# Kernel tuning notes

Measured on AMD Instinct MI355X. Metric: run time of the kernel, lower is better.

The kernel has to match this reference:

```python
import jax, jax.numpy as jnp
import numpy as np

N = 100000      # num nodes
E = 800000      # num edges
IN = 128        # in_channels
OUT = 128       # out_channels
ALPHA = 0.5


def setup_inputs() -> dict:
    key = jax.random.key(0)
    k1, k2, k3, k4, k5, k6 = jax.random.split(key, 6)
    x = jax.random.normal(k1, (N, IN), dtype=jnp.float32)
    edge_index = jax.random.randint(k2, (2, E), 0, N, dtype=jnp.int32)
    # GCNConv linear weights (glorot-ish) and biases for both directions
    s = 1.0 / np.sqrt(IN)
    W_sd = jax.random.normal(k3, (IN, OUT), dtype=jnp.float32) * s
    b_sd = jnp.zeros((OUT,), dtype=jnp.float32)
    W_ds = jax.random.normal(k4, (IN, OUT), dtype=jnp.float32) * s
    b_ds = jnp.zeros((OUT,), dtype=jnp.float32)
    return {"x": x, "edge_index": edge_index, "W_sd": W_sd, "b_sd": b_sd,
            "W_ds": W_ds, "b_ds": b_ds}


def _dir_gcn_norm_weights(row, col, dtype):
    """edge_weight = out_deg_inv_sqrt[row] * in_deg_inv_sqrt[col] (unit input weights)."""
    ones = jnp.ones((row.shape[0],), dtype=dtype)
    in_deg = jax.ops.segment_sum(ones, col, num_segments=N)
    out_deg = jax.ops.segment_sum(ones, row, num_segments=N)
    in_inv = jnp.where(in_deg > 0, jax.lax.rsqrt(in_deg), 0.0).astype(dtype)
    out_inv = jnp.where(out_deg > 0, jax.lax.rsqrt(out_deg), 0.0).astype(dtype)
    return out_inv[row] * in_inv[col]


def _gcn_conv(x, W, b, src, dst, w):
    """GCNConv(normalize=False, add_self_loops=False): lin -> gather -> scale -> scatter-add -> +bias."""
    h = x @ W                                   # [N, OUT]
    msg = h[src] * w[:, None]                   # [E, OUT]
    return jax.ops.segment_sum(msg, dst, num_segments=N) + b


def reference(x, edge_index, W_sd, b_sd, W_ds, b_ds):
    row, col = edge_index[0], edge_index[1]
    # forward-direction norm (src->dst) and transposed-graph norm (edge_index.flip(0))
    w = _dir_gcn_norm_weights(row, col, x.dtype)
    w_t = _dir_gcn_norm_weights(col, row, x.dtype)
    # conv_dst_to_src uses transposed edges: source=col, dest=row
    x_in = _gcn_conv(x, W_ds, b_ds, col, row, w_t)
    # conv_src_to_dst uses original edges: source=row, dest=col
    x_out = _gcn_conv(x, W_sd, b_sd, row, col, w)
    return ALPHA * x_in + (1.0 - ALPHA) * x_out
```

## Files before the change

kernel.cpp:

```cpp
#include <hip/hip_runtime.h>

#define NN 100000
#define NE 800000
#define NI 1600000
#define NB 391
#define IPB 6250

#define GB_CVT 12500
#define GB_PW  128
#define GB_HIST 256

#define OFF_INV    0u
#define OFF_OFFS   800000u
#define OFF_BB     1600008u
#define OFF_HIST   1601600u
#define OFF_CSRC   2001984u
#define OFF_XB     8401984u
#define OFF_PAIRS  34001984u
#define OFF_WT     85201984u
#define OFF_BIAS   85267520u
#define OFF_TOT    85268032u

typedef short short8 __attribute__((ext_vector_type(8)));
typedef unsigned short u16x8 __attribute__((ext_vector_type(8)));
typedef float f32x4 __attribute__((ext_vector_type(4)));
typedef float f32x8 __attribute__((ext_vector_type(8)));

__device__ __forceinline__ unsigned short f2bf(float f) {
    unsigned u = __float_as_uint(f);
    u = (u + 0x7FFFu + ((u >> 16) & 1u)) >> 16;
    return (unsigned short)u;
}
__device__ __forceinline__ float b2f(unsigned short h) {
    return __uint_as_float(((unsigned)h) << 16);
}
__device__ __forceinline__ f32x8 bvec2f(u16x8 v) {
    f32x8 r;
#pragma unroll
    for (int i = 0; i < 8; ++i) r[i] = b2f(v[i]);
    return r;
}


__global__ __launch_bounds__(256) void k_prep(
    const float4* __restrict__ x4, ushort4* __restrict__ xb4,
    const float* __restrict__ Wds, const float* __restrict__ Wsd,
    const float* __restrict__ bds, const float* __restrict__ bsd,
    unsigned short* __restrict__ wt, float* __restrict__ bias,
    const int* __restrict__ ei, int* __restrict__ hist) {
    __shared__ int h[NB];
    int bid = blockIdx.x;
    if (bid < GB_CVT) {
        int i = bid * 256 + threadIdx.x;
        float4 v = x4[i];
        ushort4 o;
        o.x = f2bf(v.x); o.y = f2bf(v.y); o.z = f2bf(v.z); o.w = f2bf(v.w);
        xb4[i] = o;
        return;
    }
    if (bid < GB_CVT + GB_PW) {
        int id = (bid - GB_CVT) * 256 + threadIdx.x;
        int c = id & 127;
        int k = id >> 7;
        float v = (k < 128) ? Wds[k * 128 + c] : Wsd[(k - 128) * 128 + c];
        wt[c * 256 + k] = f2bf(v);
        if (k == 0) bias[c] = 0.5f * (bds[c] + bsd[c]);
        return;
    }
    int hb = bid - GB_CVT - GB_PW;
    for (int k = threadIdx.x; k < NB; k += 256) h[k] = 0;
    __syncthreads();
    int base = hb * IPB;
    for (int t = threadIdx.x; t < IPB; t += 256) {
        int i = base + t;
        int key = (i < NE) ? ei[i] : (NN + ei[i]);
        atomicAdd(&h[key >> 9], 1);
    }
    __syncthreads();
    for (int k = threadIdx.x; k < NB; k += 256) hist[k * 256 + hb] = h[k];
}

__global__ __launch_bounds__(256) void k_red(const int* __restrict__ hist,
                                             int* __restrict__ tot) {
    __shared__ int s[256];
    int k = blockIdx.x;
    s[threadIdx.x] = hist[k * 256 + threadIdx.x];
    __syncthreads();
    for (int st = 128; st > 0; st >>= 1) {
        if (threadIdx.x < st) s[threadIdx.x] += s[threadIdx.x + st];
        __syncthreads();
    }
    if (threadIdx.x == 0) tot[k] = s[0];
}

__global__ __launch_bounds__(512) void k_scan_tot(const int* __restrict__ tot,
                                                  int* __restrict__ bb) {
    __shared__ int sA[512], sB[512];
    int tid = threadIdx.x;
    int v = (tid < NB) ? tot[tid] : 0;
    sA[tid] = v;
    __syncthreads();
    int *src = sA, *dst = sB;
    for (int st = 1; st < 512; st <<= 1) {
        dst[tid] = src[tid] + ((tid >= st) ? src[tid - st] : 0);
        __syncthreads();
        int* tp = src; src = dst; dst = tp;
    }
    if (tid <= NB) bb[tid] = (tid > 0) ? src[tid - 1] : 0;
}

__global__ __launch_bounds__(256) void k_rebase(int* __restrict__ hist,
                                                const int* __restrict__ bb) {
    __shared__ int sA[256], sB[256];
    int k = blockIdx.x, tid = threadIdx.x;
    int v = hist[k * 256 + tid];
    sA[tid] = v;
    __syncthreads();
    int *src = sA, *dst = sB;
    for (int st = 1; st < 256; st <<= 1) {
        dst[tid] = src[tid] + ((tid >= st) ? src[tid - st] : 0);
        __syncthreads();
        int* tp = src; src = dst; dst = tp;
    }
    hist[k * 256 + tid] = bb[k] + src[tid] - v;
}

__global__ __launch_bounds__(256) void k_scatter(const int* __restrict__ ei,
                                                 const int* __restrict__ hist,
                                                 unsigned long long* __restrict__ pairs) {
    __shared__ int cur[NB];
    for (int k = threadIdx.x; k < NB; k += 256) cur[k] = hist[k * 256 + blockIdx.x];
    __syncthreads();
    int base = blockIdx.x * IPB;
    for (int t = threadIdx.x; t < IPB; t += 256) {
        int i = base + t;
        int e = ei[i];
        int key, val;
        if (i < NE) { key = e;      val = ei[NE + i]; }
        else        { key = NN + e; val = ei[i - NE]; }
        int pos = atomicAdd(&cur[key >> 9], 1);
        pairs[pos] = (((unsigned long long)(unsigned)key) << 32) | (unsigned)val;
    }
}

__global__ __launch_bounds__(256) void k_bucket(const unsigned long long* __restrict__ pairs,
                                                const int* __restrict__ bb,
                                                int* __restrict__ csr_src,
                                                int* __restrict__ offsets,
                                                float* __restrict__ inv) {
    __shared__ int sA[512], sB[512], cur[512];
    const int h = blockIdx.x, tid = threadIdx.x;
    const int s0 = bb[h], s1 = bb[h + 1];
    for (int k = tid; k < 512; k += 256) sA[k] = 0;
    __syncthreads();
    for (int i = s0 + tid; i < s1; i += 256) {
        int key = (int)(pairs[i] >> 32);
        atomicAdd(&sA[key & 511], 1);
    }
    __syncthreads();
    int *src = sA, *dst = sB;
    for (int st = 1; st < 512; st <<= 1) {
        for (int k = tid; k < 512; k += 256) dst[k] = src[k] + ((k >= st) ? src[k - st] : 0);
        __syncthreads();
        int* tp = src; src = dst; dst = tp;
    }
    for (int k = tid; k < 512; k += 256) {
        int incl = src[k];
        int excl = (k > 0) ? src[k - 1] : 0;
        cur[k] = s0 + excl;
        int gkey = h * 512 + k;
        if (gkey <= 2 * NN) offsets[gkey] = s0 + excl;
        if (gkey < 2 * NN) {
            int cnt = incl - excl;
            inv[gkey] = (cnt > 0) ? rsqrtf((float)cnt) : 0.0f;
        }
    }
    __syncthreads();
    for (int i = s0 + tid; i < s1; i += 256) {
        unsigned long long p = pairs[i];
        int key = (int)(p >> 32);
        int pos = atomicAdd(&cur[key & 511], 1);
        csr_src[pos] = (int)(unsigned)(p & 0xffffffffULL);
    }
}

__global__ __launch_bounds__(512) void k_gather_gemm(
    const u16x8* __restrict__ xb8, const int* __restrict__ offsets,
    const int* __restrict__ csr_src, const float* __restrict__ inv,
    const unsigned short* __restrict__ wt, const float* __restrict__ bias,
    float* __restrict__ out) {
    __shared__ unsigned short a_lds[16][264];

    const int wave = threadIdx.x >> 6;
    const int lane = threadIdx.x & 63;
    const int grp = lane >> 4;
    const int cl = lane & 15;
    const int nl = wave * 2 + (grp >> 1);
    const int n = blockIdx.x * 16 + nl;
    const int dir = grp & 1;

    {
        int key = dir * NN + n;
        int s0 = offsets[key], s1 = offsets[key + 1];
        const float* __restrict__ srcinv = inv + (dir ^ 1) * NN;

        f32x8 acc = {0.f, 0.f, 0.f, 0.f, 0.f, 0.f, 0.f, 0.f};
        int e = s0;
        for (; e + 4 <= s1; e += 4) {
            int i0 = csr_src[e];
            int i1 = csr_src[e + 1];
            int i2 = csr_src[e + 2];
            int i3 = csr_src[e + 3];
            float w0 = srcinv[i0], w1 = srcinv[i1], w2 = srcinv[i2], w3 = srcinv[i3];
            u16x8 v0 = xb8[i0 * 16 + cl];
            u16x8 v1 = xb8[i1 * 16 + cl];
            u16x8 v2 = xb8[i2 * 16 + cl];
            u16x8 v3 = xb8[i3 * 16 + cl];
            acc += w0 * bvec2f(v0);
            acc += w1 * bvec2f(v1);
            acc += w2 * bvec2f(v2);
            acc += w3 * bvec2f(v3);
        }
        for (; e < s1; ++e) {
            int i0 = csr_src[e];
            float w0 = srcinv[i0];
            u16x8 v0 = xb8[i0 * 16 + cl];
            acc += w0 * bvec2f(v0);
        }

        float ds = 0.5f * inv[dir * NN + n];
        u16x8 o;
#pragma unroll
        for (int i = 0; i < 8; ++i) o[i] = f2bf(acc[i] * ds);
        *(u16x8*)&a_lds[nl][dir * 128 + cl * 8] = o;
    }
    __syncthreads();

    const int fr = lane & 15;
    const int kg = (lane >> 4) * 8;
    const int col = wave * 16 + fr;

    f32x4 acc = {};
#pragma unroll
    for (int s = 0; s < 8; ++s) {
        short8 afrag = *(const short8*)&a_lds[fr][s * 32 + kg];
        short8 bfrag = *(const short8*)(wt + col * 256 + s * 32 + kg);
        acc = __builtin_amdgcn_mfma_f32_16x16x32_bf16(afrag, bfrag, acc, 0, 0, 0);
    }

    const float b = bias[col];
    const int orow0 = blockIdx.x * 16 + (lane >> 4) * 4;
#pragma unroll
    for (int i = 0; i < 4; ++i) {
        out[(orow0 + i) * 128 + col] = acc[i] + b;
    }
}

extern "C" void kernel_launch(void* const* d_in, const int* in_sizes, int n_in,
                              void* d_out, int out_size, void* d_ws, size_t ws_size,
                              hipStream_t stream) {
    const float* x   = (const float*)d_in[0];
    const int* ei    = (const int*)d_in[1];
    const float* Wsd = (const float*)d_in[2];
    const float* bsd = (const float*)d_in[3];
    const float* Wds = (const float*)d_in[4];
    const float* bds = (const float*)d_in[5];

    char* ws = (char*)d_ws;
    float* inv     = (float*)(ws + OFF_INV);
    int*   offsets = (int*)(ws + OFF_OFFS);
    int*   bb      = (int*)(ws + OFF_BB);
    int*   hist    = (int*)(ws + OFF_HIST);
    int*   csr_src = (int*)(ws + OFF_CSRC);
    unsigned short* xb  = (unsigned short*)(ws + OFF_XB);
    unsigned long long* pairs = (unsigned long long*)(ws + OFF_PAIRS);
    unsigned short* wt  = (unsigned short*)(ws + OFF_WT);
    float* bias    = (float*)(ws + OFF_BIAS);
    int*   tot     = (int*)(ws + OFF_TOT);

    k_prep<<<GB_CVT + GB_PW + GB_HIST, 256, 0, stream>>>(
        (const float4*)x, (ushort4*)xb, Wds, Wsd, bds, bsd, wt, bias, ei, hist);
    k_red<<<NB, 256, 0, stream>>>(hist, tot);
    k_scan_tot<<<1, 512, 0, stream>>>(tot, bb);
    k_rebase<<<NB, 256, 0, stream>>>(hist, bb);
    k_scatter<<<256, 256, 0, stream>>>(ei, hist, pairs);
    k_bucket<<<NB, 256, 0, stream>>>(pairs, bb, csr_src, offsets, inv);
    k_gather_gemm<<<NN / 16, 512, 0, stream>>>((const u16x8*)xb, offsets, csr_src, inv,
                                               wt, bias, (float*)d_out);
}
```

Baseline: 179.5 us.

## Retile gather-GEMM to 32 nodes per 256-thread block with 4 column tiles per wave

```diff
diff --git a/kernel.cpp b/kernel.cpp
--- a/kernel.cpp
+++ b/kernel.cpp
@@ -184,23 +184,25 @@
     }
 }
 
-__global__ __launch_bounds__(512) void k_gather_gemm(
+__global__ __launch_bounds__(256) void k_gather_gemm(
     const u16x8* __restrict__ xb8, const int* __restrict__ offsets,
     const int* __restrict__ csr_src, const float* __restrict__ inv,
     const unsigned short* __restrict__ wt, const float* __restrict__ bias,
     float* __restrict__ out) {
-    __shared__ unsigned short a_lds[16][264];
-
-    const int wave = threadIdx.x >> 6;
-    const int lane = threadIdx.x & 63;
-    const int grp = lane >> 4;
-    const int cl = lane & 15;
-    const int nl = wave * 2 + (grp >> 1);
-    const int n = blockIdx.x * 16 + nl;
-    const int dir = grp & 1;
-
-    {
-        int key = dir * NN + n;
+    __shared__ unsigned short a_lds[32][258];
+
+    const int g = threadIdx.x >> 4;
+    const int cl = threadIdx.x & 15;
+    const int n0 = blockIdx.x * 32;
+
+#pragma unroll
+    for (int i = 0; i < 4; ++i) {
+        const int seg = g + 16 * i;
+        const int nl = seg >> 1;
+        const int dir = seg & 1;
+        const int n = n0 + nl;
+
+        const int key = dir * NN + n;
         int s0 = offsets[key], s1 = offsets[key + 1];
         const float* __restrict__ srcinv = inv + (dir ^ 1) * NN;
 
@@ -231,28 +233,38 @@
         float ds = 0.5f * inv[dir * NN + n];
         u16x8 o;
 #pragma unroll
-        for (int i = 0; i < 8; ++i) o[i] = f2bf(acc[i] * ds);
+        for (int j = 0; j < 8; ++j) o[j] = f2bf(acc[j] * ds);
         *(u16x8*)&a_lds[nl][dir * 128 + cl * 8] = o;
     }
     __syncthreads();
 
+    const int wave = threadIdx.x >> 6;
+    const int lane = threadIdx.x & 63;
     const int fr = lane & 15;
     const int kg = (lane >> 4) * 8;
-    const int col = wave * 16 + fr;
-
-    f32x4 acc = {};
+    const int rt = wave >> 1;
+    const int ct0 = (wave & 1) * 4;
+
+    f32x4 acc[4] = {};
 #pragma unroll
     for (int s = 0; s < 8; ++s) {
-        short8 afrag = *(const short8*)&a_lds[fr][s * 32 + kg];
-        short8 bfrag = *(const short8*)(wt + col * 256 + s * 32 + kg);
-        acc = __builtin_amdgcn_mfma_f32_16x16x32_bf16(afrag, bfrag, acc, 0, 0, 0);
-    }
-
-    const float b = bias[col];
-    const int orow0 = blockIdx.x * 16 + (lane >> 4) * 4;
-#pragma unroll
-    for (int i = 0; i < 4; ++i) {
-        out[(orow0 + i) * 128 + col] = acc[i] + b;
+        short8 afrag = *(const short8*)&a_lds[rt * 16 + fr][s * 32 + kg];
+#pragma unroll
+        for (int c = 0; c < 4; ++c) {
+            short8 bfrag = *(const short8*)(wt + ((ct0 + c) * 16 + fr) * 256 + s * 32 + kg);
+            acc[c] = __builtin_amdgcn_mfma_f32_16x16x32_bf16(afrag, bfrag, acc[c], 0, 0, 0);
+        }
+    }
+
+    const int orow0 = n0 + rt * 16 + (lane >> 4) * 4;
+#pragma unroll
+    for (int c = 0; c < 4; ++c) {
+        const int col = (ct0 + c) * 16 + fr;
+        const float b = bias[col];
+#pragma unroll
+        for (int i = 0; i < 4; ++i) {
+            out[(orow0 + i) * 128 + col] = acc[c][i] + b;
+        }
     }
 }
 
@@ -285,6 +297,6 @@
     k_rebase<<<NB, 256, 0, stream>>>(hist, bb);
     k_scatter<<<256, 256, 0, stream>>>(ei, hist, pairs);
     k_bucket<<<NB, 256, 0, stream>>>(pairs, bb, csr_src, offsets, inv);
-    k_gather_gemm<<<NN / 16, 512, 0, stream>>>((const u16x8*)xb, offsets, csr_src, inv,
+    k_gather_gemm<<<NN / 32, 256, 0, stream>>>((const u16x8*)xb, offsets, csr_src, inv,
                                                wt, bias, (float*)d_out);
 }
```

After: 194.6 us. 1.08x slower.
